# Kernel tuning notes

Hardware: AMD Instinct MI355X
Metric: run time of the kernel (lower is better)

Reference implementation:

```python
import jax, jax.numpy as jnp
import numpy as np

B, T, C = 4, 2048, 1024
H = 16
D = C // H  # 64

def setup_inputs() -> dict:
    key = jax.random.key(0)
    k1, k2, k3, k4, k5 = jax.random.split(key, 5)
    s = 0.02
    return {
        "x": jax.random.normal(k1, (B, T, C), dtype=jnp.float32),
        "Wqkv": jax.random.normal(k2, (C, 3 * C), dtype=jnp.float32) * s,
        "bqkv": jnp.zeros((3 * C,), dtype=jnp.float32),
        "Wout": jax.random.normal(k3, (C, C), dtype=jnp.float32) * s,
        "bout": jnp.zeros((C,), dtype=jnp.float32),
    }

def reference(x, Wqkv, bqkv, Wout, bout):
    b, t, c = x.shape
    scale = D ** -0.5
    qkv = x @ Wqkv + bqkv                      # [B,T,3C]
    qkv = qkv.reshape(b, t, 3, H, D)
    q = qkv[:, :, 0].transpose(0, 2, 1, 3)     # [B,H,T,D]
    k = qkv[:, :, 1].transpose(0, 2, 1, 3)
    v = qkv[:, :, 2].transpose(0, 2, 1, 3)
    att = jnp.einsum('bhqd,bhkd->bhqk', q, k) * scale
    causal = jnp.tril(jnp.ones((t, t), dtype=bool))
    att = jnp.where(causal, att, -jnp.inf)
    att = jax.nn.softmax(att, axis=-1)
    y = jnp.einsum('bhqk,bhkd->bhqd', att, v)  # [B,H,T,D]
    y = y.transpose(0, 2, 1, 3).reshape(b, t, c)
    return y @ Wout + bout
```

## Files before the change

### kernel.cpp

```cpp
#include <hip/hip_runtime.h>
#include <hip/hip_bf16.h>


using f32x4  = __attribute__((ext_vector_type(4))) float;
using f32x16 = __attribute__((ext_vector_type(16))) float;
using s16x8  = __attribute__((ext_vector_type(8))) short;
using s16x4  = __attribute__((ext_vector_type(4))) short;

#define MFMA16(a, b, c) __builtin_amdgcn_mfma_f32_16x16x32_bf16(a, b, c, 0, 0, 0)
#define MFMA32(a, b, c) __builtin_amdgcn_mfma_f32_32x32x16_bf16(a, b, c, 0, 0, 0)

__device__ __forceinline__ unsigned short f2bf(float f) {
    unsigned u = __builtin_bit_cast(unsigned, f);
    u += 0x7fffu + ((u >> 16) & 1u);
    return (unsigned short)(u >> 16);
}

__device__ __forceinline__ void gl_lds16(const void* g, void* l) {
    __builtin_amdgcn_global_load_lds(
        (const __attribute__((address_space(1))) void*)g,
        (__attribute__((address_space(3))) void*)l, 16, 0, 0);
}

#define VMCNT(N) asm volatile("s_waitcnt vmcnt(" #N ")" ::: "memory")
#define RBAR()   __builtin_amdgcn_s_barrier()

__global__ __launch_bounds__(256) void cvt_x(const float* __restrict__ x,
                                             unsigned short* __restrict__ xb, int n4) {
    int i = blockIdx.x * 256 + threadIdx.x;
    if (i < n4) {
        f32x4 v = ((const f32x4*)x)[i];
        s16x4 o;
        o[0] = (short)f2bf(v[0]); o[1] = (short)f2bf(v[1]);
        o[2] = (short)f2bf(v[2]); o[3] = (short)f2bf(v[3]);
        ((s16x4*)xb)[i] = o;
    }
}

__global__ __launch_bounds__(256) void cvt_tr(const float* __restrict__ W,
                                              unsigned short* __restrict__ Wt,
                                              int R, int Cc) {
    __shared__ unsigned short tile[64][72];
    const int r0 = blockIdx.x * 64, c0 = blockIdx.y * 64;
    const int tid = threadIdx.x;
    const int r = tid >> 4, c4 = (tid & 15) * 4;
#pragma unroll
    for (int i = 0; i < 4; ++i) {
        f32x4 v = *(const f32x4*)(W + (size_t)(r0 + r + i * 16) * Cc + c0 + c4);
#pragma unroll
        for (int j = 0; j < 4; ++j) tile[r + i * 16][c4 + j] = f2bf(v[j]);
    }
    __syncthreads();
#pragma unroll
    for (int i = 0; i < 4; ++i) {
        s16x4 o;
#pragma unroll
        for (int j = 0; j < 4; ++j) o[j] = (short)tile[c4 + j][r + i * 16];
        *(s16x4*)(Wt + (size_t)(c0 + r + i * 16) * R + r0 + c4) = o;
    }
}

template <int MODE>
__global__ __launch_bounds__(256, 2) void gemm_bt(
    const unsigned short* __restrict__ A, const unsigned short* __restrict__ Bt,
    const float* __restrict__ bias,
    unsigned short* __restrict__ qp, unsigned short* __restrict__ kp,
    unsigned short* __restrict__ vtp, float* __restrict__ outp,
    int M, int N, int K)
{
    __shared__ unsigned short As[2][128 * 64];
    __shared__ unsigned short Bs[2][128 * 64];

    const int tid  = threadIdx.x;
    const int lane = tid & 63, w = tid >> 6;
    const int wm = w >> 1, wn = w & 1;
    const int g = lane >> 4, li = lane & 15;
    const int m0 = blockIdx.x * 128, n0 = blockIdx.y * 128;

    const int srow = lane >> 3;
    const int ssw  = ((lane & 7) ^ srow) * 8;

    f32x4 acc[4][4] = {};

    auto STAGE = [&](int buf, int k0) {
#pragma unroll
        for (int j = 0; j < 4; ++j) {
            const int rr = w * 32 + j * 8;
            gl_lds16(A  + (size_t)(m0 + rr + srow) * K + k0 + ssw, &As[buf][rr * 64]);
            gl_lds16(Bt + (size_t)(n0 + rr + srow) * K + k0 + ssw, &Bs[buf][rr * 64]);
        }
    };

    STAGE(0, 0);
    VMCNT(0);
    __syncthreads();

    const int nt = K >> 6;
    int cur = 0;
    for (int t = 0; t < nt; ++t) {
        if (t + 1 < nt) STAGE(cur ^ 1, (t + 1) << 6);

        s16x8 af[4][2], bf[4][2];
#pragma unroll
        for (int i = 0; i < 4; ++i) {
            const int ra = wm * 64 + i * 16 + li;
            const int rb = wn * 64 + i * 16 + li;
#pragma unroll
            for (int kk = 0; kk < 2; ++kk) {
                af[i][kk] = *(const s16x8*)(
                    &As[cur][ra * 64 + (((kk * 4 + g) ^ (ra & 7)) << 3)]);
                bf[i][kk] = *(const s16x8*)(
                    &Bs[cur][rb * 64 + (((kk * 4 + g) ^ (rb & 7)) << 3)]);
            }
        }

        __builtin_amdgcn_s_setprio(1);
#pragma unroll
        for (int kk = 0; kk < 2; ++kk)
#pragma unroll
            for (int mi = 0; mi < 4; ++mi)
#pragma unroll
                for (int ni = 0; ni < 4; ++ni)
                    acc[mi][ni] = MFMA16(af[mi][kk], bf[ni][kk], acc[mi][ni]);
        __builtin_amdgcn_s_setprio(0);

        VMCNT(0);
        __syncthreads();
        cur ^= 1;
    }

#pragma unroll
    for (int ni = 0; ni < 4; ++ni) {
        const int n = n0 + wn * 64 + ni * 16 + li;
        const float bv = bias[n];
        const int s = n >> 10, h = (n >> 6) & 15, d = n & 63;
#pragma unroll
        for (int mi = 0; mi < 4; ++mi) {
            const int mB = m0 + wm * 64 + mi * 16 + g * 4;
            float v0 = acc[mi][ni][0] + bv, v1 = acc[mi][ni][1] + bv;
            float v2 = acc[mi][ni][2] + bv, v3 = acc[mi][ni][3] + bv;
            if (MODE == 0) {
                const int b = mB >> 11, tt = mB & 2047;
                if (s == 2) {
                    unsigned pk01, pk23;
                    asm("v_cvt_pk_bf16_f32 %0, %1, %2" : "=v"(pk01) : "v"(v0), "v"(v1));
                    asm("v_cvt_pk_bf16_f32 %0, %1, %2" : "=v"(pk23) : "v"(v2), "v"(v3));
                    unsigned short* dst = vtp + ((size_t)(b * 16 + h) * 64 + d) * 2048 + tt;
                    *(unsigned*)dst = pk01;
                    *(unsigned*)(dst + 2) = pk23;
                } else {
                    const float sc2 = (s == 0) ? 0.1803368801111143f : 1.0f;
                    unsigned short* dst =
                        ((s == 0) ? qp : kp) + ((size_t)(b * 16 + h) * 2048 + tt) * 64 + d;
                    dst[0]   = f2bf(v0 * sc2);
                    dst[64]  = f2bf(v1 * sc2);
                    dst[128] = f2bf(v2 * sc2);
                    dst[192] = f2bf(v3 * sc2);
                }
            } else {
                float* dst = outp + (size_t)mB * N + n;
                dst[0] = v0; dst[N] = v1; dst[2 * N] = v2; dst[3 * N] = v3;
            }
        }
    }
}

__global__ __launch_bounds__(256, 4) void attn_k(
    const unsigned short* __restrict__ qbuf,
    const unsigned short* __restrict__ kbuf,
    const unsigned short* __restrict__ vtbuf,
    unsigned short* __restrict__ ybuf)
{
    __shared__ unsigned short Ks[2][4096];
    __shared__ unsigned short Vs[2][4096];

    const int tid  = threadIdx.x;
    const int lane = tid & 63, w = tid >> 6;
    const int l31 = lane & 31;
    const int h5  = lane >> 5;

    const int id   = blockIdx.x;
    const int slot = id >> 3;
    const int bh   = (id & 7) * 8 + (slot & 7);
    const int bx   = slot >> 3;
    const int qtA  = 31 - bx, qtB = bx;

    const int Tw    = (w < 2) ? qtA : qtB;
    const int wrow0 = Tw * 64 + (w & 1) * 32;

    const unsigned short* qb  = qbuf  + (size_t)bh * 131072;
    const unsigned short* kb  = kbuf  + (size_t)bh * 131072;
    const unsigned short* vtb = vtbuf + (size_t)bh * 131072;
    const int b = bh >> 4, h = bh & 15;

    const int srow = lane >> 3;
    const int ssw  = ((lane & 7) ^ srow) * 8;

    auto STAGE = [&](int p, int kbase) {
#pragma unroll
        for (int jj = 0; jj < 2; ++jj) {
            const int j = w * 2 + jj, row = j * 8 + srow;
            gl_lds16(kb  + (size_t)(kbase + row) * 64 + ssw, &Ks[p][j * 512]);
            gl_lds16(vtb + (size_t)row * 2048 + kbase + ssw, &Vs[p][j * 512]);
        }
    };

    const int qrow = wrow0 + l31;
    const unsigned short* qr = qb + (size_t)qrow * 64 + h5 * 8;
    s16x8 qf[4];
#pragma unroll
    for (int s = 0; s < 4; ++s) qf[s] = *(const s16x8*)(qr + s * 16);

    f32x16 O0 = {}, O1 = {};
    float lsum = 0.f;

    const int nkb = qtA + 1;
    STAGE(0, 0);

    for (int t = 0; t < nkb; ++t) {
        const int p = t & 1;
        const int kbase = t * 64;
        const bool more = (t + 1 < nkb);

        if (more) {
            STAGE(p ^ 1, kbase + 64);
            VMCNT(4);
        } else {
            VMCNT(0);
        }
        RBAR();

        if (t <= Tw) {
            f32x16 s0 = {}, s1 = {};
            __builtin_amdgcn_s_setprio(1);
#pragma unroll
            for (int s = 0; s < 4; ++s) {
                const int c = s * 2 + h5;
                const int sw = (c ^ (l31 & 7)) << 3;
                s16x8 kf0 = *(const s16x8*)(&Ks[p][l31 * 64 + sw]);
                s16x8 kf1 = *(const s16x8*)(&Ks[p][(32 + l31) * 64 + sw]);
                s0 = MFMA32(kf0, qf[s], s0);
                s1 = MFMA32(kf1, qf[s], s1);
            }
            __builtin_amdgcn_s_setprio(0);

            if (kbase + 63 > wrow0) {
#pragma unroll
                for (int r = 0; r < 16; ++r) {
                    const int k0 = kbase + (r & 3) + 8 * (r >> 2) + 4 * h5;
                    if (k0 > qrow)      s0[r] = -1e30f;
                    if (k0 + 32 > qrow) s1[r] = -1e30f;
                }
            }

            float rsa = 0.f, rsb = 0.f, rsc = 0.f, rsd = 0.f;
#pragma unroll
            for (int r = 0; r < 16; r += 2) {
                s0[r]     = __builtin_amdgcn_exp2f(s0[r]);
                s0[r + 1] = __builtin_amdgcn_exp2f(s0[r + 1]);
                s1[r]     = __builtin_amdgcn_exp2f(s1[r]);
                s1[r + 1] = __builtin_amdgcn_exp2f(s1[r + 1]);
                rsa += s0[r]; rsb += s0[r + 1];
                rsc += s1[r]; rsd += s1[r + 1];
            }
            float rs = (rsa + rsb) + (rsc + rsd);
            rs += __shfl_xor(rs, 32);
            lsum += rs;

            s16x8 pa[4];
#pragma unroll
            for (int G = 0; G < 2; ++G) {
#pragma unroll
                for (int half = 0; half < 2; ++half) {
                    const int bse = half * 8;
                    unsigned w0, w1, w2, w3;
                    if (G == 0) {
                        asm("v_cvt_pk_bf16_f32 %0, %1, %2" : "=v"(w0) : "v"(s0[bse + 0]), "v"(s0[bse + 1]));
                        asm("v_cvt_pk_bf16_f32 %0, %1, %2" : "=v"(w1) : "v"(s0[bse + 2]), "v"(s0[bse + 3]));
                        asm("v_cvt_pk_bf16_f32 %0, %1, %2" : "=v"(w2) : "v"(s0[bse + 4]), "v"(s0[bse + 5]));
                        asm("v_cvt_pk_bf16_f32 %0, %1, %2" : "=v"(w3) : "v"(s0[bse + 6]), "v"(s0[bse + 7]));
                    } else {
                        asm("v_cvt_pk_bf16_f32 %0, %1, %2" : "=v"(w0) : "v"(s1[bse + 0]), "v"(s1[bse + 1]));
                        asm("v_cvt_pk_bf16_f32 %0, %1, %2" : "=v"(w1) : "v"(s1[bse + 2]), "v"(s1[bse + 3]));
                        asm("v_cvt_pk_bf16_f32 %0, %1, %2" : "=v"(w2) : "v"(s1[bse + 4]), "v"(s1[bse + 5]));
                        asm("v_cvt_pk_bf16_f32 %0, %1, %2" : "=v"(w3) : "v"(s1[bse + 6]), "v"(s1[bse + 7]));
                    }
                    auto r02 = __builtin_amdgcn_permlane32_swap(w0, w2, false, false);
                    auto r13 = __builtin_amdgcn_permlane32_swap(w1, w3, false, false);
                    union { unsigned u[4]; s16x8 v; } P;
                    P.u[0] = r02[0]; P.u[1] = r13[0];
                    P.u[2] = r02[1]; P.u[3] = r13[1];
                    pa[G * 2 + half] = P.v;
                }
            }

            __builtin_amdgcn_s_setprio(1);
#pragma unroll
            for (int kg = 0; kg < 4; ++kg) {
                const int c = kg * 2 + h5;
                const int sw = (c ^ (l31 & 7)) << 3;
                s16x8 vf0 = *(const s16x8*)(&Vs[p][l31 * 64 + sw]);
                s16x8 vf1 = *(const s16x8*)(&Vs[p][(32 + l31) * 64 + sw]);
                O0 = MFMA32(pa[kg], vf0, O0);
                O1 = MFMA32(pa[kg], vf1, O1);
            }
            __builtin_amdgcn_s_setprio(0);
        }

        if (more) RBAR();
    }

    const float linv = __builtin_amdgcn_rcpf(lsum);
#pragma unroll
    for (int r = 0; r < 16; ++r) {
        const int qi = (r & 3) + 8 * (r >> 2) + 4 * h5;
        const float lr = __shfl(linv, qi);
        const int row = wrow0 + qi;
        const size_t base = ((size_t)(b * 2048 + row)) * 1024 + h * 64;
        ybuf[base + l31]      = f2bf(O0[r] * lr);
        ybuf[base + 32 + l31] = f2bf(O1[r] * lr);
    }
}

extern "C" void kernel_launch(void* const* d_in, const int* in_sizes, int n_in,
                              void* d_out, int out_size, void* d_ws, size_t ws_size,
                              hipStream_t stream)
{
    const float* x    = (const float*)d_in[0];
    const float* Wqkv = (const float*)d_in[1];
    const float* bqkv = (const float*)d_in[2];
    const float* Wout = (const float*)d_in[3];
    const float* bout = (const float*)d_in[4];

    unsigned short* ws0 = (unsigned short*)d_ws;
    unsigned short* ws1 = ws0 + (size_t)8388608;
    unsigned short* ws2 = ws0 + (size_t)2 * 8388608;
    unsigned short* ws3 = ws0 + (size_t)3 * 8388608;

    unsigned short* xbf   = (unsigned short*)d_out;
    unsigned short* WqkvT = xbf + (size_t)8388608;

    cvt_x<<<8192, 256, 0, stream>>>(x, xbf, 2097152);
    cvt_tr<<<dim3(16, 48), 256, 0, stream>>>(Wqkv, WqkvT, 1024, 3072);
    gemm_bt<0><<<dim3(64, 24), 256, 0, stream>>>(
        xbf, WqkvT, bqkv, ws0, ws1, ws2, nullptr, 8192, 3072, 1024);
    attn_k<<<1024, 256, 0, stream>>>(ws0, ws1, ws2, ws3);
    cvt_tr<<<dim3(16, 16), 256, 0, stream>>>(Wout, ws0, 1024, 1024);
    gemm_bt<1><<<dim3(64, 8), 256, 0, stream>>>(
        ws3, ws0, bout, nullptr, nullptr, nullptr, (float*)d_out, 8192, 1024, 1024);
}
```

Before: 161.0 us.

## Triple-buffer GEMM with BK=32 tiles and two-stage-ahead prefetch

The GEMM moves from a double-buffered K=64 tile to a triple-buffered K=32 tile. Loads are issued two stages ahead and waited on with a partial vmcnt, so global-to-LDS transfers overlap compute more deeply. Smaller LDS buffers allow launch bounds of 3 blocks per SM for higher occupancy. In exchange there are twice as many loop iterations and barriers, and each barrier covers half as many MFMAs. The new swizzle also has to stay bank-conflict free.

```diff
diff --git a/kernel.cpp b/kernel.cpp
--- a/kernel.cpp
+++ b/kernel.cpp
@@ -61,15 +61,15 @@
 }
 
 template <int MODE>
-__global__ __launch_bounds__(256, 2) void gemm_bt(
+__global__ __launch_bounds__(256, 3) void gemm_bt(
     const unsigned short* __restrict__ A, const unsigned short* __restrict__ Bt,
     const float* __restrict__ bias,
     unsigned short* __restrict__ qp, unsigned short* __restrict__ kp,
     unsigned short* __restrict__ vtp, float* __restrict__ outp,
     int M, int N, int K)
 {
-    __shared__ unsigned short As[2][128 * 64];
-    __shared__ unsigned short Bs[2][128 * 64];
+    __shared__ unsigned short As[3][128 * 32];
+    __shared__ unsigned short Bs[3][128 * 32];
 
     const int tid  = threadIdx.x;
     const int lane = tid & 63, w = tid >> 6;
@@ -77,56 +77,53 @@
     const int g = lane >> 4, li = lane & 15;
     const int m0 = blockIdx.x * 128, n0 = blockIdx.y * 128;
 
-    const int srow = lane >> 3;
-    const int ssw  = ((lane & 7) ^ srow) * 8;
+    const int srow   = lane >> 2;
+    const int schunk = ((lane & 3) ^ ((lane >> 3) & 3)) * 8;
 
     f32x4 acc[4][4] = {};
 
-    auto STAGE = [&](int buf, int k0) {
-#pragma unroll
-        for (int j = 0; j < 4; ++j) {
-            const int rr = w * 32 + j * 8;
-            gl_lds16(A  + (size_t)(m0 + rr + srow) * K + k0 + ssw, &As[buf][rr * 64]);
-            gl_lds16(Bt + (size_t)(n0 + rr + srow) * K + k0 + ssw, &Bs[buf][rr * 64]);
+    auto STAGE = [&](int buf, int t) {
+        const int k0 = t << 5;
+#pragma unroll
+        for (int j = 0; j < 2; ++j) {
+            const int rr = j * 64 + w * 16;
+            gl_lds16(A  + (size_t)(m0 + rr + srow) * K + k0 + schunk, &As[buf][rr * 32]);
+            gl_lds16(Bt + (size_t)(n0 + rr + srow) * K + k0 + schunk, &Bs[buf][rr * 32]);
         }
     };
 
     STAGE(0, 0);
-    VMCNT(0);
-    __syncthreads();
-
-    const int nt = K >> 6;
-    int cur = 0;
+    STAGE(1, 1);
+    VMCNT(4);
+    RBAR();
+
+    const int nt = K >> 5;
     for (int t = 0; t < nt; ++t) {
-        if (t + 1 < nt) STAGE(cur ^ 1, (t + 1) << 6);
-
-        s16x8 af[4][2], bf[4][2];
+        const int cur = t % 3;
+        const bool pre = (t + 2 < nt);
+        if (pre) STAGE((t + 2) % 3, t + 2);
+
+        s16x8 af[4], bf[4];
 #pragma unroll
         for (int i = 0; i < 4; ++i) {
             const int ra = wm * 64 + i * 16 + li;
             const int rb = wn * 64 + i * 16 + li;
-#pragma unroll
-            for (int kk = 0; kk < 2; ++kk) {
-                af[i][kk] = *(const s16x8*)(
-                    &As[cur][ra * 64 + (((kk * 4 + g) ^ (ra & 7)) << 3)]);
-                bf[i][kk] = *(const s16x8*)(
-                    &Bs[cur][rb * 64 + (((kk * 4 + g) ^ (rb & 7)) << 3)]);
-            }
+            af[i] = *(const s16x8*)(&As[cur][ra * 32 + ((g ^ ((ra >> 1) & 3)) << 3)]);
+            bf[i] = *(const s16x8*)(&Bs[cur][rb * 32 + ((g ^ ((rb >> 1) & 3)) << 3)]);
         }
 
         __builtin_amdgcn_s_setprio(1);
 #pragma unroll
-        for (int kk = 0; kk < 2; ++kk)
-#pragma unroll
-            for (int mi = 0; mi < 4; ++mi)
-#pragma unroll
-                for (int ni = 0; ni < 4; ++ni)
-                    acc[mi][ni] = MFMA16(af[mi][kk], bf[ni][kk], acc[mi][ni]);
+        for (int mi = 0; mi < 4; ++mi)
+#pragma unroll
+            for (int ni = 0; ni < 4; ++ni)
+                acc[mi][ni] = MFMA16(af[mi], bf[ni], acc[mi][ni]);
         __builtin_amdgcn_s_setprio(0);
 
-        VMCNT(0);
-        __syncthreads();
-        cur ^= 1;
+        if (t + 1 < nt) {
+            if (pre) VMCNT(4); else VMCNT(0);
+            RBAR();
+        }
     }
 
 #pragma unroll
```

New measurement: 167.5 us. 1.04x slower.

## Split causal attention work evenly between wave pairs with split-K merge

Applied to the files above, without the earlier changes.

Each block previously handled two query tiles (a long one and a short one), with all four waves walking the long tile's key range, so the waves on the short tile sat idle for most iterations. Now each wave pair streams its own K/V tiles into separate LDS buffers. Pair 1 finishes the short tile, writes it out, then takes over the upper half of the long tile's key blocks. The two partial results are merged through LDS at the end. This doubles LDS use and lowers launch_bounds occupancy from 4 to 2 blocks per CU, and it relies on the unnormalized exp2 softmax having no running max, so partial sums can simply be added.

```diff
diff --git a/kernel.cpp b/kernel.cpp
--- a/kernel.cpp
+++ b/kernel.cpp
@@ -165,17 +165,18 @@
     }
 }
 
-__global__ __launch_bounds__(256, 4) void attn_k(
+__global__ __launch_bounds__(256, 2) void attn_k(
     const unsigned short* __restrict__ qbuf,
     const unsigned short* __restrict__ kbuf,
     const unsigned short* __restrict__ vtbuf,
     unsigned short* __restrict__ ybuf)
 {
-    __shared__ unsigned short Ks[2][4096];
-    __shared__ unsigned short Vs[2][4096];
+    __shared__ unsigned short Ksh[2][2][4096];
+    __shared__ unsigned short Vsh[2][2][4096];
 
     const int tid  = threadIdx.x;
     const int lane = tid & 63, w = tid >> 6;
+    const int pair = w >> 1, pw = w & 1;
     const int l31 = lane & 31;
     const int h5  = lane >> 5;
 
@@ -185,9 +186,6 @@
     const int bx   = slot >> 3;
     const int qtA  = 31 - bx, qtB = bx;
 
-    const int Tw    = (w < 2) ? qtA : qtB;
-    const int wrow0 = Tw * 64 + (w & 1) * 32;
-
     const unsigned short* qb  = qbuf  + (size_t)bh * 131072;
     const unsigned short* kb  = kbuf  + (size_t)bh * 131072;
     const unsigned short* vtb = vtbuf + (size_t)bh * 131072;
@@ -196,49 +194,67 @@
     const int srow = lane >> 3;
     const int ssw  = ((lane & 7) ^ srow) * 8;
 
-    auto STAGE = [&](int p, int kbase) {
-#pragma unroll
-        for (int jj = 0; jj < 2; ++jj) {
-            const int j = w * 2 + jj, row = j * 8 + srow;
-            gl_lds16(kb  + (size_t)(kbase + row) * 64 + ssw, &Ks[p][j * 512]);
-            gl_lds16(vtb + (size_t)row * 2048 + kbase + ssw, &Vs[p][j * 512]);
+    auto STAGE = [&](int buf, int t) {
+        const int kb0 = t * 64;
+#pragma unroll
+        for (int j = 0; j < 4; ++j) {
+            const int br = j * 16 + pw * 8;
+            gl_lds16(kb  + (size_t)(kb0 + br + srow) * 64 + ssw, &Ksh[pair][buf][br * 64]);
+            gl_lds16(vtb + (size_t)(br + srow) * 2048 + kb0 + ssw, &Vsh[pair][buf][br * 64]);
         }
     };
 
-    const int qrow = wrow0 + l31;
-    const unsigned short* qr = qb + (size_t)qrow * 64 + h5 * 8;
-    s16x8 qf[4];
-#pragma unroll
-    for (int s = 0; s < 4; ++s) qf[s] = *(const s16x8*)(qr + s * 16);
+    int wrow0 = ((pair == 0) ? qtA : qtB) * 64 + pw * 32;
+    int qrow  = wrow0 + l31;
+
+    const int qrowA = qtA * 64 + pw * 32 + l31;
+    s16x8 qf[4], qfA2[4];
+    {
+        const unsigned short* qr  = qb + (size_t)qrow * 64 + h5 * 8;
+        const unsigned short* qra = qb + (size_t)qrowA * 64 + h5 * 8;
+#pragma unroll
+        for (int s = 0; s < 4; ++s) {
+            qf[s]   = *(const s16x8*)(qr + s * 16);
+            qfA2[s] = *(const s16x8*)(qra + s * 16);
+        }
+    }
 
     f32x16 O0 = {}, O1 = {};
     float lsum = 0.f;
 
-    const int nkb = qtA + 1;
-    STAGE(0, 0);
-
-    for (int t = 0; t < nkb; ++t) {
-        const int p = t & 1;
-        const int kbase = t * 64;
-        const bool more = (t + 1 < nkb);
-
-        if (more) {
-            STAGE(p ^ 1, kbase + 64);
-            VMCNT(4);
+    const int lastI = (pair == 0) ? 16 : 15;
+    auto tOf = [&](int i) -> int {
+        return (pair == 0) ? i : ((i <= bx) ? i : (16 + i - bx));
+    };
+
+    STAGE(0, tOf(0));
+
+    int bufc = 0;
+    for (int i = 0; i < 17; ++i) {
+        const bool haveT    = (i <= lastI);
+        const bool haveNext = (i + 1 <= lastI);
+        if (haveNext) {
+            STAGE(bufc ^ 1, tOf(i + 1));
+            VMCNT(8);
         } else {
             VMCNT(0);
         }
         RBAR();
 
-        if (t <= Tw) {
+        if (haveT) {
+            const int t = tOf(i);
+            const int kbase = t * 64;
+            const unsigned short* Kp = &Ksh[pair][bufc][0];
+            const unsigned short* Vp = &Vsh[pair][bufc][0];
+
             f32x16 s0 = {}, s1 = {};
             __builtin_amdgcn_s_setprio(1);
 #pragma unroll
             for (int s = 0; s < 4; ++s) {
                 const int c = s * 2 + h5;
                 const int sw = (c ^ (l31 & 7)) << 3;
-                s16x8 kf0 = *(const s16x8*)(&Ks[p][l31 * 64 + sw]);
-                s16x8 kf1 = *(const s16x8*)(&Ks[p][(32 + l31) * 64 + sw]);
+                s16x8 kf0 = *(const s16x8*)(Kp + l31 * 64 + sw);
+                s16x8 kf1 = *(const s16x8*)(Kp + (32 + l31) * 64 + sw);
                 s0 = MFMA32(kf0, qf[s], s0);
                 s1 = MFMA32(kf1, qf[s], s1);
             }
@@ -299,26 +315,69 @@
             for (int kg = 0; kg < 4; ++kg) {
                 const int c = kg * 2 + h5;
                 const int sw = (c ^ (l31 & 7)) << 3;
-                s16x8 vf0 = *(const s16x8*)(&Vs[p][l31 * 64 + sw]);
-                s16x8 vf1 = *(const s16x8*)(&Vs[p][(32 + l31) * 64 + sw]);
+                s16x8 vf0 = *(const s16x8*)(Vp + l31 * 64 + sw);
+                s16x8 vf1 = *(const s16x8*)(Vp + (32 + l31) * 64 + sw);
                 O0 = MFMA32(pa[kg], vf0, O0);
                 O1 = MFMA32(pa[kg], vf1, O1);
             }
             __builtin_amdgcn_s_setprio(0);
-        }
-
-        if (more) RBAR();
-    }
-
-    const float linv = __builtin_amdgcn_rcpf(lsum);
-#pragma unroll
-    for (int r = 0; r < 16; ++r) {
-        const int qi = (r & 3) + 8 * (r >> 2) + 4 * h5;
-        const float lr = __shfl(linv, qi);
-        const int row = wrow0 + qi;
-        const size_t base = ((size_t)(b * 2048 + row)) * 1024 + h * 64;
-        ybuf[base + l31]      = f2bf(O0[r] * lr);
-        ybuf[base + 32 + l31] = f2bf(O1[r] * lr);
+
+            if (pair == 1 && i == bx) {
+                const float linv = __builtin_amdgcn_rcpf(lsum);
+#pragma unroll
+                for (int r = 0; r < 16; ++r) {
+                    const int qi = (r & 3) + 8 * (r >> 2) + 4 * h5;
+                    const float lr = __shfl(linv, qi);
+                    const int row = wrow0 + qi;
+                    const size_t base = ((size_t)(b * 2048 + row)) * 1024 + h * 64;
+                    ybuf[base + l31]      = f2bf(O0[r] * lr);
+                    ybuf[base + 32 + l31] = f2bf(O1[r] * lr);
+                }
+#pragma unroll
+                for (int r = 0; r < 16; ++r) { O0[r] = 0.f; O1[r] = 0.f; }
+                lsum = 0.f;
+                wrow0 = qtA * 64 + pw * 32;
+                qrow  = wrow0 + l31;
+#pragma unroll
+                for (int s = 0; s < 4; ++s) qf[s] = qfA2[s];
+            }
+        }
+
+        RBAR();
+        bufc ^= 1;
+    }
+
+    __syncthreads();
+    float* mrg = (float*)&Ksh[0][0][0];
+    if (pair == 1) {
+        float* basep = mrg + pw * (33 * 64);
+#pragma unroll
+        for (int r = 0; r < 16; ++r) {
+            basep[r * 64 + lane]        = O0[r];
+            basep[(16 + r) * 64 + lane] = O1[r];
+        }
+        basep[32 * 64 + lane] = lsum;
+    }
+    __syncthreads();
+    if (pair == 0) {
+        const float* basep = mrg + pw * (33 * 64);
+#pragma unroll
+        for (int r = 0; r < 16; ++r) {
+            O0[r] += basep[r * 64 + lane];
+            O1[r] += basep[(16 + r) * 64 + lane];
+        }
+        lsum += basep[32 * 64 + lane];
+
+        const float linv = __builtin_amdgcn_rcpf(lsum);
+#pragma unroll
+        for (int r = 0; r < 16; ++r) {
+            const int qi = (r & 3) + 8 * (r >> 2) + 4 * h5;
+            const float lr = __shfl(linv, qi);
+            const int row = wrow0 + qi;
+            const size_t base = ((size_t)(b * 2048 + row)) * 1024 + h * 64;
+            ybuf[base + l31]      = f2bf(O0[r] * lr);
+            ybuf[base + 32 + l31] = f2bf(O1[r] * lr);
+        }
     }
 }
 
```

Result: slower. 172.8 us (+7.3%).
